# Performance work log

Measured on AMD Instinct MI355X. Metric: run time of the kernel, lower is better.

## Reference

```python
import math
import jax, jax.numpy as jnp
import numpy as np

B, S, IN_DIM, D_MODEL, L, T_Y = 16, 512, 64, 64, 32, 256
T_X = T_Y + L - 1
RIDGE = 0.01
THRESH = 0.005


def _pos_encoding(seq_len, d):
    pos = jnp.arange(seq_len, dtype=jnp.float32)[:, None]
    div = jnp.exp(jnp.arange(0, d, 2, dtype=jnp.float32) * (-(math.log(10000.0) / d)))
    ang = pos * div  # [S, d/2]
    pe = jnp.zeros((seq_len, d), dtype=jnp.float32)
    pe = pe.at[:, 0::2].set(jnp.sin(ang)).at[:, 1::2].set(jnp.cos(ang))
    return pe


def _layernorm(h, gamma, beta, eps=1e-5):
    mu = jnp.mean(h, axis=-1, keepdims=True)
    var = jnp.mean((h - mu) ** 2, axis=-1, keepdims=True)
    return (h - mu) * jax.lax.rsqrt(var + eps) * gamma + beta


def setup_inputs() -> dict:
    key = jax.random.key(0)
    ks = jax.random.split(key, 8)
    return {
        "fps": jax.random.normal(ks[0], (B, S, IN_DIM), dtype=jnp.float32),
        "x": jax.random.normal(ks[1], (B, S, T_X), dtype=jnp.float32),
        "y": jax.random.normal(ks[2], (B, S, T_Y), dtype=jnp.float32),
        "sample_steps": jax.random.randint(ks[3], (5,), 10, S),
        "W1": jax.random.normal(ks[4], (IN_DIM, 256), dtype=jnp.float32) / math.sqrt(IN_DIM),
        "b1": jnp.zeros((256,), dtype=jnp.float32),
        "gamma": jnp.ones((256,), dtype=jnp.float32),
        "beta": jnp.zeros((256,), dtype=jnp.float32),
        "W2": jax.random.normal(ks[5], (256, D_MODEL), dtype=jnp.float32) / math.sqrt(256.0),
        "b2": jnp.zeros((D_MODEL,), dtype=jnp.float32),
        "Wq": jax.random.normal(ks[6], (D_MODEL, D_MODEL), dtype=jnp.float32) / math.sqrt(D_MODEL),
        "bq": jnp.zeros((D_MODEL,), dtype=jnp.float32),
        "Wk": jax.random.normal(ks[7], (D_MODEL, D_MODEL), dtype=jnp.float32) / math.sqrt(D_MODEL),
        "bk": jnp.zeros((D_MODEL,), dtype=jnp.float32),
    }


def reference(fps, x, y, sample_steps, W1, b1, gamma, beta, W2, b2, Wq, bq, Wk, bk):
    batch, seq_len, _ = fps.shape
    d = Wq.shape[0]
    t_y = y.shape[-1]
    filt = x.shape[-1] - t_y + 1  # L

    # encoder: Linear -> LayerNorm -> Tanh -> Linear -> Tanh
    h = _layernorm(fps @ W1 + b1, gamma, beta)
    e_orig = jnp.tanh(jnp.tanh(h) @ W2 + b2)  # [B,S,d]
    e = e_orig + 0.05 * _pos_encoding(seq_len, d)[None]

    q = e @ Wq + bq
    k = e @ Wk + bk
    scores = jnp.einsum('bsd,btd->bst', q, k) / math.sqrt(d)
    causal = jnp.triu(jnp.ones((seq_len, seq_len), dtype=bool), 1)
    scores = jnp.where(causal[None], -1e9, scores)
    alpha = jax.nn.softmax(scores * 2.0, axis=-1)  # [B,S,S]

    # sliding windows: X[b,s] = unfold(x[b,s], L, 1)[:T_y] -> [T_y, L]
    win = jnp.arange(t_y)[:, None] + jnp.arange(filt)[None, :]
    X = x[:, :, win]  # [B,S,T_y,L]

    # per-source gram / cross contributions
    G = jnp.einsum('bstl,bstm->bslm', X, X)  # [B,S,L,L]
    C = jnp.einsum('bstl,bst->bsl', X, y)    # [B,S,L]

    w = alpha[:, sample_steps, :]            # [B,T,S]
    wm = jnp.where(w > THRESH, w, 0.0)

    gram = jnp.einsum('bts,bslm->btlm', wm, G) + RIDGE * jnp.eye(filt, dtype=x.dtype)
    cross = jnp.einsum('bts,bsl->btl', wm, C)
    wt_hat = jnp.linalg.solve(gram, cross[..., None])[..., 0]  # [B,T,L]

    Xt = X[:, sample_steps]  # [B,T,T_y,L]
    yt = y[:, sample_steps]  # [B,T,T_y]
    pred = jnp.einsum('btkl,btl->btk', Xt, wt_hat)
    loss_bt = jnp.mean((yt - pred) ** 2, axis=-1)  # [B,T]

    valid = jnp.any(wm > 0.0, axis=-1)  # [B,T]
    total = jnp.sum(jnp.where(valid, loss_bt, 0.0))
    n = jnp.maximum(jnp.sum(valid.astype(jnp.int32)), 1)
    loss = total / n
    return loss, alpha, e_orig
```

## Files before the change

kernel.cpp:

```cpp
#include <hip/hip_runtime.h>
#include <math.h>

#define BB 16
#define SS 512
#define INDIM 64
#define DMODEL 64
#define HID 256
#define FILT 32
#define TYY 256
#define TXX 287
#define NT 5
#define RIDGEF 0.01f
#define THRESHF 0.005f
#define GRAMN 1088
#define GRAMTOT (BB * NT * GRAMN)

__device__ __forceinline__ float ftanh(float v)
{
    float vc = fminf(fmaxf(v, -15.f), 15.f);
    float e = __expf(2.f * vc);
    return (e - 1.f) / (e + 1.f);
}

__global__ __launch_bounds__(256) void k_mlp(
    const float* __restrict__ fps, const float* __restrict__ W1, const float* __restrict__ b1,
    const float* __restrict__ gamma, const float* __restrict__ beta,
    const float* __restrict__ W2, const float* __restrict__ b2,
    const float* __restrict__ Wq, const float* __restrict__ bq,
    const float* __restrict__ Wk, const float* __restrict__ bk,
    float* __restrict__ e_out, float* __restrict__ q_out, float* __restrict__ kT_out,
    float* __restrict__ gram, int* __restrict__ ctrs)
{
    const int row0 = blockIdx.x << 3;
    const int tid = threadIdx.x;
    const int wid = tid >> 6, lane = tid & 63;

    if (blockIdx.x < GRAMTOT / 256) {
        gram[(size_t)blockIdx.x * 256 + tid] = 0.f;
    } else if (blockIdx.x == GRAMTOT / 256 && tid < 4) {
        ctrs[tid] = 0;
    }

    __shared__ float fr[8][INDIM];
    __shared__ float th4[8][HID];
    __shared__ float ee4[4][DMODEL];
    __shared__ float part4[4][4][DMODEL];
    __shared__ float partk4[4][4][DMODEL];
    __shared__ float wred[4][8][2];

    { int r = tid >> 6, i = tid & 63;
      fr[r][i]     = fps[(row0 + r) * INDIM + i];
      fr[r + 4][i] = fps[(row0 + r + 4) * INDIM + i]; }
    __syncthreads();

    float h[8];
    float b1v = b1[tid];
    #pragma unroll
    for (int r = 0; r < 8; ++r) h[r] = b1v;
    for (int i = 0; i < INDIM; ++i) {
        float w = W1[i * HID + tid];
        #pragma unroll
        for (int r = 0; r < 8; ++r) h[r] = fmaf(fr[r][i], w, h[r]);
    }

    float s1[8], s2[8];
    #pragma unroll
    for (int r = 0; r < 8; ++r) { s1[r] = h[r]; s2[r] = h[r] * h[r]; }
    #pragma unroll
    for (int off = 1; off < 64; off <<= 1) {
        #pragma unroll
        for (int r = 0; r < 8; ++r) {
            s1[r] += __shfl_xor(s1[r], off);
            s2[r] += __shfl_xor(s2[r], off);
        }
    }
    if (lane == 0) {
        #pragma unroll
        for (int r = 0; r < 8; ++r) { wred[wid][r][0] = s1[r]; wred[wid][r][1] = s2[r]; }
    }
    __syncthreads();
    float gm = gamma[tid], bt = beta[tid];
    #pragma unroll
    for (int r = 0; r < 8; ++r) {
        float t1 = wred[0][r][0] + wred[1][r][0] + wred[2][r][0] + wred[3][r][0];
        float t2 = wred[0][r][1] + wred[1][r][1] + wred[2][r][1] + wred[3][r][1];
        float mu = t1 * (1.0f / HID);
        float var = t2 * (1.0f / HID) - mu * mu;
        float hn = (h[r] - mu) * rsqrtf(var + 1e-5f) * gm + bt;
        th4[r][tid] = ftanh(hn);
    }
    __syncthreads();

    #pragma unroll
    for (int half = 0; half < 2; ++half) {
        const int rbase = half * 4;
        { int p = tid >> 6, j = tid & 63;
          float acc[4] = {0.f, 0.f, 0.f, 0.f};
          for (int i = p * 64; i < p * 64 + 64; ++i) {
              float w = W2[i * DMODEL + j];
              #pragma unroll
              for (int r = 0; r < 4; ++r) acc[r] = fmaf(th4[rbase + r][i], w, acc[r]);
          }
          #pragma unroll
          for (int r = 0; r < 4; ++r) part4[p][r][j] = acc[r];
        }
        __syncthreads();
        { int r = tid >> 6, j = tid & 63;
          float e = part4[0][r][j] + part4[1][r][j] + part4[2][r][j] + part4[3][r][j] + b2[j];
          float eo = ftanh(e);
          int row = row0 + rbase + r;
          int s = row & (SS - 1);
          e_out[(size_t)row * DMODEL + j] = eo;
          float div = __expf(-(float)(j & ~1) * 0.14391156831212787f);
          float ang = (float)s * div;
          float pe = (j & 1) ? __cosf(ang) : __sinf(ang);
          ee4[r][j] = eo + 0.05f * pe;
        }
        __syncthreads();
        { int p = tid >> 6, j = tid & 63;
          float aq[4] = {0.f,0.f,0.f,0.f}, ak[4] = {0.f,0.f,0.f,0.f};
          for (int i = p * 16; i < p * 16 + 16; ++i) {
              float wqv = Wq[i * DMODEL + j];
              float wkv = Wk[i * DMODEL + j];
              #pragma unroll
              for (int r = 0; r < 4; ++r) {
                  aq[r] = fmaf(ee4[r][i], wqv, aq[r]);
                  ak[r] = fmaf(ee4[r][i], wkv, ak[r]);
              }
          }
          #pragma unroll
          for (int r = 0; r < 4; ++r) { part4[p][r][j] = aq[r]; partk4[p][r][j] = ak[r]; }
        }
        __syncthreads();
        { int r = tid >> 6, j = tid & 63;
          float qv = part4[0][r][j] + part4[1][r][j] + part4[2][r][j] + part4[3][r][j] + bq[j];
          float kv = partk4[0][r][j] + partk4[1][r][j] + partk4[2][r][j] + partk4[3][r][j] + bk[j];
          int row = row0 + rbase + r;
          int b = row >> 9, s = row & (SS - 1);
          q_out[(size_t)row * DMODEL + j] = qv;
          kT_out[(size_t)(b * DMODEL + j) * SS + s] = kv;
        }
        __syncthreads();
    }
}

__global__ __launch_bounds__(256) void k_attn(
    const float* __restrict__ q, const float* __restrict__ kT,
    float* __restrict__ alpha)
{
    const int blk = blockIdx.x;
    const int b = blk >> 6;
    const int t0 = (blk & 63) << 3;
    const int t7 = t0 + 7;
    const int tid = threadIdx.x;
    const int wave = tid >> 6, lane = tid & 63;

    __shared__ float qt[8 * DMODEL];
    __shared__ float redm[8][4];

    { size_t qb = (size_t)(b * SS + t0) * DMODEL;
      qt[tid] = q[qb + tid];
      qt[tid + 256] = q[qb + tid + 256]; }
    __syncthreads();

    const float* kTb = kT + (size_t)b * DMODEL * SS;
    const int s0 = tid, s1 = tid + 256;
    float a0[8] = {0,0,0,0,0,0,0,0}, a1[8] = {0,0,0,0,0,0,0,0};
    if (t7 >= 256) {
        for (int d = 0; d < DMODEL; ++d) {
            float k0 = kTb[d * SS + s0];
            float k1 = kTb[d * SS + s1];
            #pragma unroll
            for (int r = 0; r < 8; ++r) {
                float qv = qt[r * DMODEL + d];
                a0[r] = fmaf(qv, k0, a0[r]);
                a1[r] = fmaf(qv, k1, a1[r]);
            }
        }
    } else {
        for (int d = 0; d < DMODEL; ++d) {
            float k0 = kTb[d * SS + s0];
            #pragma unroll
            for (int r = 0; r < 8; ++r)
                a0[r] = fmaf(qt[r * DMODEL + d], k0, a0[r]);
        }
    }
    float lg0[8], lg1[8];
    #pragma unroll
    for (int r = 0; r < 8; ++r) {
        int tr = t0 + r;
        lg0[r] = (s0 <= tr) ? 0.25f * a0[r] : -INFINITY;
        lg1[r] = (s1 <= tr) ? 0.25f * a1[r] : -INFINITY;
    }
    float mr[8];
    #pragma unroll
    for (int r = 0; r < 8; ++r) {
        float m = fmaxf(lg0[r], lg1[r]);
        #pragma unroll
        for (int off = 32; off > 0; off >>= 1) m = fmaxf(m, __shfl_xor(m, off));
        if (lane == 0) redm[r][wave] = m;
    }
    __syncthreads();
    #pragma unroll
    for (int r = 0; r < 8; ++r)
        mr[r] = fmaxf(fmaxf(redm[r][0], redm[r][1]), fmaxf(redm[r][2], redm[r][3]));
    __syncthreads();
    float ex0[8], ex1[8], sr[8];
    #pragma unroll
    for (int r = 0; r < 8; ++r) {
        ex0[r] = __expf(lg0[r] - mr[r]);
        ex1[r] = __expf(lg1[r] - mr[r]);
        float sm = ex0[r] + ex1[r];
        #pragma unroll
        for (int off = 32; off > 0; off >>= 1) sm += __shfl_xor(sm, off);
        if (lane == 0) redm[r][wave] = sm;
    }
    __syncthreads();
    #pragma unroll
    for (int r = 0; r < 8; ++r)
        sr[r] = redm[r][0] + redm[r][1] + redm[r][2] + redm[r][3];
    #pragma unroll
    for (int r = 0; r < 8; ++r) {
        float inv = 1.0f / sr[r];
        size_t base = (size_t)(b * SS + t0 + r) * SS;
        alpha[base + s0] = ex0[r] * inv;
        alpha[base + s1] = ex1[r] * inv;
    }
}

__global__ __launch_bounds__(256) void k_gpart(
    const float* __restrict__ x, const float* __restrict__ y,
    const int* __restrict__ steps, const float* __restrict__ alpha,
    float* __restrict__ gram, int C, int CS)
{
    const int b = blockIdx.x / C;
    const int chunk = blockIdx.x % C;
    const int tid = threadIdx.x;
    const int lane = tid & 63, wid = tid >> 6;

    __shared__ __align__(16) float xs[288];
    __shared__ __align__(16) float ys[256];
    __shared__ float Gs[1056];
    __shared__ float crossL[32];
    __shared__ float wv[NT * 64];
    __shared__ float wtot[NT];
    __shared__ int sl[64];
    __shared__ int nselS;
    __shared__ int stS[NT];
    __shared__ float redA[4][33];
    __shared__ float redB[4][33];

    if (tid < NT) stS[tid] = steps[tid];
    if (tid < 32) Gs[tid * 33 + 32] = 0.f;
    __syncthreads();

    for (int idx = tid; idx < NT * CS; idx += 256) {
        int t = idx / CS, si = idx % CS;
        float a = alpha[(size_t)(b * SS + stS[t]) * SS + chunk * CS + si];
        wv[t * 64 + si] = (a > THRESHF) ? a : 0.f;
    }
    __syncthreads();
    if (tid < NT) {
        float s = 0.f;
        for (int si = 0; si < CS; ++si) s += wv[tid * 64 + si];
        wtot[tid] = s;
    }
    if (wid == 0) {
        float m = 0.f;
        if (lane < CS)
            m = wv[lane] + wv[64 + lane] + wv[128 + lane] + wv[192 + lane] + wv[256 + lane];
        unsigned long long mask = __ballot(m > 0.f);
        if (m > 0.f) {
            int pos = __popcll(mask & ((1ull << lane) - 1ull));
            sl[pos] = lane;
        }
        if (lane == 0) nselS = __popcll(mask);
    }
    __syncthreads();
    const int nsel = nselS;

    float acc[NT][5];
    #pragma unroll
    for (int t = 0; t < NT; ++t) {
        #pragma unroll
        for (int r = 0; r < 5; ++r) acc[t][r] = 0.f;
    }

    float rx0 = 0.f, rx1 = 0.f, ry = 0.f;
    if (nsel > 0) {
        int sg = chunk * CS + sl[0];
        const float* xr = x + (size_t)(b * SS + sg) * TXX;
        const float* yr = y + (size_t)(b * SS + sg) * TYY;
        rx0 = xr[tid];
        if (tid < 31) rx1 = xr[256 + tid];
        ry = yr[tid];
    }

    for (int i = 0; i < nsel; ++i) {
        xs[tid] = rx0;
        if (tid < 31) xs[256 + tid] = rx1;
        ys[tid] = ry;
        const int sl_cur = sl[i];
        __syncthreads();

        if (i + 1 < nsel) {
            int sg = chunk * CS + sl[i + 1];
            const float* xr = x + (size_t)(b * SS + sg) * TXX;
            const float* yr = y + (size_t)(b * SS + sg) * TYY;
            rx0 = xr[tid];
            if (tid < 31) rx1 = xr[256 + tid];
            ry = yr[tid];
        }

        { int l = tid & 31, p = tid >> 5;
          const float4* xk4 = (const float4*)(xs + (p << 5));
          const float4* yk4 = (const float4*)(ys + (p << 5));
          float c = 0.f, a = 0.f;
          #pragma unroll
          for (int j = 0; j < 8; ++j) {
              float4 xk = xk4[j];
              float4 yk = yk4[j];
              int kb = (p << 5) + (j << 2);
              float x0 = xs[kb + l],     x1 = xs[kb + 1 + l];
              float x2 = xs[kb + 2 + l], x3 = xs[kb + 3 + l];
              c = fmaf(x0, yk.x, c); a = fmaf(xk.x, x0, a);
              c = fmaf(x1, yk.y, c); a = fmaf(xk.y, x1, a);
              c = fmaf(x2, yk.z, c); a = fmaf(xk.z, x2, a);
              c = fmaf(x3, yk.w, c); a = fmaf(xk.w, x3, a);
          }
          c += __shfl_xor(c, 32);
          a += __shfl_xor(a, 32);
          if (lane < 32) { redA[wid][l] = c; redB[wid][l] = a; }
        }
        __syncthreads();

        if (tid < 32)
            crossL[tid] = redA[0][tid] + redA[1][tid] + redA[2][tid] + redA[3][tid];

        { int jj = lane & 31;
          #pragma unroll
          for (int pass = 0; pass < 4; ++pass) {
              int dd = 2 * (wid + 4 * pass) + (lane >> 5);
              float g0 = redB[0][dd] + redB[1][dd] + redB[2][dd] + redB[3][dd];
              float dlt = 0.f;
              if (jj > 0 && jj + dd < 32)
                  dlt = xs[jj + 255] * xs[jj + 255 + dd]
                      - xs[jj - 1] * xs[jj - 1 + dd];
              #pragma unroll
              for (int off = 1; off < 32; off <<= 1) {
                  float tsh = __shfl_up(dlt, off, 32);
                  if (jj >= off) dlt += tsh;
              }
              if (jj + dd < 32) {
                  float gval = g0 + dlt;
                  Gs[jj * 33 + jj + dd] = gval;
                  Gs[(jj + dd) * 33 + jj] = gval;
              }
          }
        }
        __syncthreads();

        { float g0 = Gs[tid], g1 = Gs[tid + 256], g2 = Gs[tid + 512], g3 = Gs[tid + 768];
          float g4 = (tid < 32) ? Gs[1024 + tid]
                   : ((tid < 64) ? crossL[tid - 32] : 0.f);
          #pragma unroll
          for (int t = 0; t < NT; ++t) {
              float w = wv[t * 64 + sl_cur];
              if (w > 0.f) {
                  acc[t][0] = fmaf(w, g0, acc[t][0]);
                  acc[t][1] = fmaf(w, g1, acc[t][1]);
                  acc[t][2] = fmaf(w, g2, acc[t][2]);
                  acc[t][3] = fmaf(w, g3, acc[t][3]);
                  acc[t][4] = fmaf(w, g4, acc[t][4]);
              }
          }
        }
    }

    #pragma unroll
    for (int t = 0; t < NT; ++t) {
        if (wtot[t] > 0.f) {
            float* gr = gram + (size_t)(b * NT + t) * GRAMN;
            #pragma unroll
            for (int r = 0; r < 4; ++r) atomicAdd(&gr[tid + 256 * r], acc[t][r]);
            if (tid < 64) atomicAdd(&gr[1024 + tid], acc[t][4]);
        }
    }
}

__global__ __launch_bounds__(256) void k_solve2(
    const float* __restrict__ x, const float* __restrict__ y,
    const int* __restrict__ steps, const float* __restrict__ alpha,
    const float* __restrict__ gram,
    int* __restrict__ ctrs, float* __restrict__ out0)
{
    const int g = blockIdx.x;
    const int b = g / NT, t = g % NT;
    const int tid = threadIdx.x;

    __shared__ float Af[1056];
    __shared__ float zs[FILT];
    __shared__ float wt[FILT];
    __shared__ float xsr[TXX + 1];
    __shared__ float red[256];
    __shared__ int step_s;
    __shared__ int anyv;

    if (tid == 0) { step_s = steps[t]; anyv = 0; }
    __syncthreads();

    const float* row = gram + (size_t)g * GRAMN;
    Af[tid] = row[tid];
    Af[tid + 256] = row[tid + 256];
    Af[tid + 512] = row[tid + 512];
    Af[tid + 768] = row[tid + 768];
    if (tid < 32) Af[1024 + tid] = row[1024 + tid];
    else if (tid < 64) zs[tid - 32] = row[1024 + tid];

    { const float* arow = alpha + (size_t)(b * SS + step_s) * SS;
      if (arow[tid] > THRESHF || arow[tid + 256] > THRESHF) anyv = 1; }
    __syncthreads();
    if (tid < 32) Af[tid * 33 + tid] += RIDGEF;
    __syncthreads();

    if (tid < 32) {
        float a[32];
        #pragma unroll
        for (int j = 0; j < 32; ++j) a[j] = Af[tid * 33 + j];
        #pragma unroll
        for (int k = 0; k < 32; ++k) {
            float akk = __shfl(a[k], k);
            float dk = sqrtf(akk);
            float ck = a[k] / dk;
            if (tid >= k) a[k] = ck;
            #pragma unroll
            for (int m = k + 1; m < 32; ++m) {
                float cm = __shfl(ck, m);
                if (tid >= m) a[m] = fmaf(-ck, cm, a[m]);
            }
        }
        #pragma unroll
        for (int j = 0; j < 32; ++j)
            if (j <= tid) Af[tid * 33 + j] = a[j];

        float zl = zs[tid];
        #pragma unroll
        for (int k = 0; k < 32; ++k) {
            float akk = __shfl(a[k], k);
            float zk = __shfl(zl, k) / akk;
            if (tid == k) zl = zk;
            else if (tid > k) zl = fmaf(-a[k], zk, zl);
        }
        #pragma unroll
        for (int k = 31; k >= 0; --k) {
            float akk = __shfl(a[k], k);
            float wk = __shfl(zl, k) / akk;
            if (tid == k) zl = wk;
            else if (tid < k) zl = fmaf(-Af[k * 33 + tid], wk, zl);
        }
        wt[tid] = zl;
    }
    __syncthreads();

    const int sstep = step_s;
    const float* xrow = x + (size_t)(b * SS + sstep) * TXX;
    for (int i = tid; i < TXX; i += 256) xsr[i] = xrow[i];
    __syncthreads();
    float pk = 0.f;
    #pragma unroll
    for (int l = 0; l < FILT; ++l) pk = fmaf(xsr[tid + l], wt[l], pk);
    float d = y[(size_t)(b * SS + sstep) * TYY + tid] - pk;
    red[tid] = d * d;
    __syncthreads();
    for (int off = 128; off > 0; off >>= 1) {
        if (tid < off) red[tid] += red[tid + off];
        __syncthreads();
    }
    if (tid == 0) {
        float lossval = red[0] * (1.0f / TYY);
        float* loss_sum = (float*)(ctrs + 2);
        if (anyv) {
            atomicAdd(loss_sum, lossval);
            atomicAdd(&ctrs[1], 1);
        }
        __threadfence();
        int prev = atomicAdd(&ctrs[0], 1);
        if (prev == BB * NT - 1) {
            float s = atomicAdd(loss_sum, 0.0f);
            int c = atomicAdd(&ctrs[1], 0);
            out0[0] = s / (float)(c > 0 ? c : 1);
        }
    }
}

extern "C" void kernel_launch(void* const* d_in, const int* in_sizes, int n_in,
                              void* d_out, int out_size, void* d_ws, size_t ws_size,
                              hipStream_t stream)
{
    const float* fps  = (const float*)d_in[0];
    const float* x    = (const float*)d_in[1];
    const float* y    = (const float*)d_in[2];
    const int* steps  = (const int*)d_in[3];
    const float* W1   = (const float*)d_in[4];
    const float* b1   = (const float*)d_in[5];
    const float* gamma= (const float*)d_in[6];
    const float* beta = (const float*)d_in[7];
    const float* W2   = (const float*)d_in[8];
    const float* b2   = (const float*)d_in[9];
    const float* Wq   = (const float*)d_in[10];
    const float* bq   = (const float*)d_in[11];
    const float* Wk   = (const float*)d_in[12];
    const float* bk   = (const float*)d_in[13];

    float* out   = (float*)d_out;
    float* alpha = out + 1;
    float* e_out = out + 1 + (size_t)BB * SS * SS;

    float* gram = (float*)d_ws;
    int*   ctrs = (int*)(gram + GRAMTOT);
    float* q    = (float*)(ctrs + 4);
    float* kT   = q + (size_t)BB * SS * DMODEL;

    const int C = 64, CS = SS / 64;

    hipLaunchKernelGGL(k_mlp, dim3(BB * SS / 8), dim3(256), 0, stream,
                       fps, W1, b1, gamma, beta, W2, b2, Wq, bq, Wk, bk,
                       e_out, q, kT, gram, ctrs);
    hipLaunchKernelGGL(k_attn, dim3(BB * (SS / 8)), dim3(256), 0, stream,
                       q, kT, alpha);
    hipLaunchKernelGGL(k_gpart, dim3(BB * C), dim3(256), 0, stream,
                       x, y, steps, alpha, gram, C, CS);
    hipLaunchKernelGGL(k_solve2, dim3(BB * NT), dim3(256), 0, stream,
                       x, y, steps, alpha, gram, ctrs, out);
}
```

Before: 191.8 us.

## Replace gram atomic accumulation with per-chunk partial buffers reduced in solve

Each k_gpart block now writes its per-chunk gram and cross contributions to its own slot in a partials buffer with plain stores, instead of atomically adding into a shared zeroed gram buffer. k_solve2 then sums the 64 chunk partials before doing the Cholesky solve, and the gram zeroing in k_mlp is removed. This is meant to remove atomic contention and the zero-init pass. In exchange every chunk now writes its full partial even when its weights are all zero, the workspace grows to about 22 MB, and the final reduction runs inside only 80 solve blocks, each reading 64 partials.

After: 213.1 us. 1.11x slower.

```diff
diff --git a/kernel.cpp b/kernel.cpp
--- a/kernel.cpp
+++ b/kernel.cpp
@@ -10,10 +10,11 @@
 #define TYY 256
 #define TXX 287
 #define NT 5
+#define NCH 64
 #define RIDGEF 0.01f
 #define THRESHF 0.005f
 #define GRAMN 1088
-#define GRAMTOT (BB * NT * GRAMN)
+#define PARTTOT ((size_t)BB * NCH * NT * GRAMN)
 
 __device__ __forceinline__ float ftanh(float v)
 {
@@ -29,15 +30,13 @@
     const float* __restrict__ Wq, const float* __restrict__ bq,
     const float* __restrict__ Wk, const float* __restrict__ bk,
     float* __restrict__ e_out, float* __restrict__ q_out, float* __restrict__ kT_out,
-    float* __restrict__ gram, int* __restrict__ ctrs)
+    int* __restrict__ ctrs)
 {
     const int row0 = blockIdx.x << 3;
     const int tid = threadIdx.x;
     const int wid = tid >> 6, lane = tid & 63;
 
-    if (blockIdx.x < GRAMTOT / 256) {
-        gram[(size_t)blockIdx.x * 256 + tid] = 0.f;
-    } else if (blockIdx.x == GRAMTOT / 256 && tid < 4) {
+    if (blockIdx.x == 0 && tid < 4) {
         ctrs[tid] = 0;
     }
 
@@ -231,7 +230,7 @@
 __global__ __launch_bounds__(256) void k_gpart(
     const float* __restrict__ x, const float* __restrict__ y,
     const int* __restrict__ steps, const float* __restrict__ alpha,
-    float* __restrict__ gram, int C, int CS)
+    float* __restrict__ part, int C, int CS)
 {
     const int b = blockIdx.x / C;
     const int chunk = blockIdx.x % C;
@@ -243,7 +242,6 @@
     __shared__ float Gs[1056];
     __shared__ float crossL[32];
     __shared__ float wv[NT * 64];
-    __shared__ float wtot[NT];
     __shared__ int sl[64];
     __shared__ int nselS;
     __shared__ int stS[NT];
@@ -260,11 +258,6 @@
         wv[t * 64 + si] = (a > THRESHF) ? a : 0.f;
     }
     __syncthreads();
-    if (tid < NT) {
-        float s = 0.f;
-        for (int si = 0; si < CS; ++si) s += wv[tid * 64 + si];
-        wtot[tid] = s;
-    }
     if (wid == 0) {
         float m = 0.f;
         if (lane < CS)
@@ -379,19 +372,17 @@
 
     #pragma unroll
     for (int t = 0; t < NT; ++t) {
-        if (wtot[t] > 0.f) {
-            float* gr = gram + (size_t)(b * NT + t) * GRAMN;
-            #pragma unroll
-            for (int r = 0; r < 4; ++r) atomicAdd(&gr[tid + 256 * r], acc[t][r]);
-            if (tid < 64) atomicAdd(&gr[1024 + tid], acc[t][4]);
-        }
+        float* gr = part + ((size_t)(b * C + chunk) * NT + t) * GRAMN;
+        #pragma unroll
+        for (int r = 0; r < 4; ++r) gr[tid + 256 * r] = acc[t][r];
+        if (tid < 64) gr[1024 + tid] = acc[t][4];
     }
 }
 
 __global__ __launch_bounds__(256) void k_solve2(
     const float* __restrict__ x, const float* __restrict__ y,
     const int* __restrict__ steps, const float* __restrict__ alpha,
-    const float* __restrict__ gram,
+    const float* __restrict__ part,
     int* __restrict__ ctrs, float* __restrict__ out0)
 {
     const int g = blockIdx.x;
@@ -409,13 +400,24 @@
     if (tid == 0) { step_s = steps[t]; anyv = 0; }
     __syncthreads();
 
-    const float* row = gram + (size_t)g * GRAMN;
-    Af[tid] = row[tid];
-    Af[tid + 256] = row[tid + 256];
-    Af[tid + 512] = row[tid + 512];
-    Af[tid + 768] = row[tid + 768];
-    if (tid < 32) Af[1024 + tid] = row[1024 + tid];
-    else if (tid < 64) zs[tid - 32] = row[1024 + tid];
+    { const float* pb = part + ((size_t)b * NCH * NT + t) * GRAMN;
+      float s0 = 0.f, s1 = 0.f, s2 = 0.f, s3 = 0.f, s4 = 0.f;
+      #pragma unroll 4
+      for (int p = 0; p < NCH; ++p) {
+          const float* rp = pb + (size_t)p * (NT * GRAMN);
+          s0 += rp[tid];
+          s1 += rp[tid + 256];
+          s2 += rp[tid + 512];
+          s3 += rp[tid + 768];
+          if (tid < 64) s4 += rp[1024 + tid];
+      }
+      Af[tid]       = s0;
+      Af[tid + 256] = s1;
+      Af[tid + 512] = s2;
+      Af[tid + 768] = s3;
+      if (tid < 32) Af[1024 + tid] = s4;
+      else if (tid < 64) zs[tid - 32] = s4;
+    }
 
     { const float* arow = alpha + (size_t)(b * SS + step_s) * SS;
       if (arow[tid] > THRESHF || arow[tid + 256] > THRESHF) anyv = 1; }
@@ -516,20 +518,20 @@
     float* alpha = out + 1;
     float* e_out = out + 1 + (size_t)BB * SS * SS;
 
-    float* gram = (float*)d_ws;
-    int*   ctrs = (int*)(gram + GRAMTOT);
+    float* part = (float*)d_ws;
+    int*   ctrs = (int*)(part + PARTTOT);
     float* q    = (float*)(ctrs + 4);
     float* kT   = q + (size_t)BB * SS * DMODEL;
 
-    const int C = 64, CS = SS / 64;
+    const int C = NCH, CS = SS / NCH;
 
     hipLaunchKernelGGL(k_mlp, dim3(BB * SS / 8), dim3(256), 0, stream,
                        fps, W1, b1, gamma, beta, W2, b2, Wq, bq, Wk, bk,
-                       e_out, q, kT, gram, ctrs);
+                       e_out, q, kT, ctrs);
     hipLaunchKernelGGL(k_attn, dim3(BB * (SS / 8)), dim3(256), 0, stream,
                        q, kT, alpha);
     hipLaunchKernelGGL(k_gpart, dim3(BB * C), dim3(256), 0, stream,
-                       x, y, steps, alpha, gram, C, CS);
+                       x, y, steps, alpha, part, C, CS);
     hipLaunchKernelGGL(k_solve2, dim3(BB * NT), dim3(256), 0, stream,
-                       x, y, steps, alpha, gram, ctrs, out);
+                       x, y, steps, alpha, part, ctrs, out);
 }
```
